# Kernel tuning notes

Hardware: AMD Instinct MI355X
Metric: run time of the kernel (lower is better)

Reference implementation:

```python
import jax, jax.numpy as jnp
import numpy as np

HISTORY = 128  # self-inclusive causal window width

def _layernorm(x, g, b, eps=1e-5):
    mu = jnp.mean(x, axis=-1, keepdims=True)
    var = jnp.var(x, axis=-1, keepdims=True)
    return (x - mu) * jax.lax.rsqrt(var + eps) * g + b

def setup_inputs() -> dict:
    key = jax.random.key(0)
    ks = jax.random.split(key, 8)
    dim, hid, B, T = 64, 256, 4, 4096
    s = lambda fan_in: 1.0 / np.sqrt(fan_in)
    return {
        "x": jax.random.normal(ks[0], (B, T, dim), jnp.float32),
        "W_in": jax.random.normal(ks[1], (dim, hid), jnp.float32) * s(dim),
        "b_in": jnp.zeros((hid,), jnp.float32),
        "W_qkv": jax.random.normal(ks[2], (hid, 3 * hid), jnp.float32) * s(hid),
        "b_qkv": jnp.zeros((3 * hid,), jnp.float32),
        "g_attn": jnp.ones((hid,), jnp.float32),
        "be_attn": jnp.zeros((hid,), jnp.float32),
        "g_mlp": jnp.ones((hid,), jnp.float32),
        "be_mlp": jnp.zeros((hid,), jnp.float32),
        "W1": jax.random.normal(ks[3], (hid, hid), jnp.float32) * s(hid),
        "b1": jnp.zeros((hid,), jnp.float32),
        "W2": jax.random.normal(ks[4], (hid, hid), jnp.float32) * s(hid),
        "b2": jnp.zeros((hid,), jnp.float32),
        "W_out": jax.random.normal(ks[5], (hid, dim), jnp.float32) * s(hid),
        "b_out": jnp.zeros((dim,), jnp.float32),
    }

def reference(x, W_in, b_in, W_qkv, b_qkv, g_attn, be_attn, g_mlp, be_mlp,
              W1, b1, W2, b2, W_out, b_out):
    B, T, _ = x.shape
    hid = W_in.shape[1]
    h = x @ W_in + b_in                                  # (B,T,hid)
    qkv = _layernorm(h, g_attn, be_attn) @ W_qkv + b_qkv
    q, k, v = jnp.split(qkv, 3, axis=-1)
    scale = 1.0 / jnp.sqrt(jnp.asarray(hid, x.dtype))
    scores = jnp.einsum('bqd,bkd->bqk', q, k) * scale    # (B,T,T)
    idx = jnp.arange(T)
    delta = idx[:, None] - idx[None, :]
    mask = (delta >= 0) & (delta <= HISTORY)             # self-inclusive window
    scores = jnp.where(mask[None], scores, jnp.finfo(x.dtype).min)
    attn = jax.nn.softmax(scores, axis=-1)
    attn_out = jnp.einsum('bqk,bkd->bqd', attn, v)
    h = h + attn_out                                     # residual (dropout=0)
    m = _layernorm(h, g_mlp, be_mlp)
    m = jax.nn.gelu(m @ W1 + b1, approximate=False) @ W2 + b2
    h = h + m
    return h @ W_out + b_out                             # (B,T,dim)
```

## Files before the change

kernel.cpp:

```cpp
#include <hip/hip_runtime.h>
#include <hip/hip_bf16.h>
#include <math.h>

typedef short bf8 __attribute__((ext_vector_type(8)));
typedef float f4  __attribute__((ext_vector_type(4)));

#define DEV static __device__ __forceinline__

DEV f4 MFMA(bf8 a, bf8 b, f4 c) { return __builtin_amdgcn_mfma_f32_16x16x32_bf16(a, b, c, 0, 0, 0); }

DEV unsigned short f2bf(float f) {
  union { float f; unsigned int u; } v; v.f = f;
  unsigned int r = v.u + 0x7FFFu + ((v.u >> 16) & 1u);
  return (unsigned short)(r >> 16);
}
DEV float bf2f(unsigned short u) {
  union { unsigned int u; float f; } v; v.u = ((unsigned int)u) << 16;
  return v.f;
}

struct P15 { const void* p[15]; };

DEV float ldin(const void* p, int i, bool bf) {
  return bf ? bf2f(((const unsigned short*)p)[i]) : ((const float*)p)[i];
}

#define PB_IN 0
#define PB_QKV 256
#define PB1 1024
#define PB2 1280
#define PB_OUT 1536
#define PGA 1600
#define PBA 1856
#define PGM 2112
#define PBM 2368

__global__ __launch_bounds__(256) void k_prep(P15 in,
    unsigned short* __restrict__ WinT, unsigned short* __restrict__ WqkvT,
    unsigned short* __restrict__ W1T, unsigned short* __restrict__ W2T,
    unsigned short* __restrict__ WoutT, float* __restrict__ par)
{
  const bool bf = (*(const unsigned int*)in.p[5]) == 0x3F803F80u;
  const int E0 = 16384;
  const int E1 = E0 + 196608;
  const int E2 = E1 + 65536;
  const int E3 = E2 + 65536;
  const int E4 = E3 + 16384;
  const int E5 = E4 + 2624;
  for (int i = blockIdx.x * 256 + threadIdx.x; i < E5; i += gridDim.x * 256) {
    if (i < E0) {
      int n = i >> 6, k = i & 63;
      WinT[i] = f2bf(ldin(in.p[1], k * 256 + n, bf));
    } else if (i < E1) {
      int j = i - E0, n = j >> 8, k = j & 255;
      WqkvT[j] = f2bf(ldin(in.p[3], k * 768 + n, bf));
    } else if (i < E2) {
      int j = i - E1, n = j >> 8, k = j & 255;
      W1T[j] = f2bf(ldin(in.p[9], k * 256 + n, bf));
    } else if (i < E3) {
      int j = i - E2, n = j >> 8, k = j & 255;
      W2T[j] = f2bf(ldin(in.p[11], k * 256 + n, bf));
    } else if (i < E4) {
      int j = i - E3, n = j >> 8, k = j & 255;
      WoutT[j] = f2bf(ldin(in.p[13], k * 64 + n, bf));
    } else {
      int j = i - E4;
      const void* src; int o;
      if (j < 256)       { src = in.p[2];  o = j; }
      else if (j < 1024) { src = in.p[4];  o = j - 256; }
      else if (j < 1280) { src = in.p[10]; o = j - 1024; }
      else if (j < 1536) { src = in.p[12]; o = j - 1280; }
      else if (j < 1600) { src = in.p[14]; o = j - 1536; }
      else if (j < 1856) { src = in.p[5];  o = j - 1600; }
      else if (j < 2112) { src = in.p[6];  o = j - 1856; }
      else if (j < 2368) { src = in.p[7];  o = j - 2112; }
      else               { src = in.p[8];  o = j - 2368; }
      par[j] = ldin(src, o, bf);
    }
  }
}

__global__ __launch_bounds__(512, 2) void k_in_qkv(const void* __restrict__ xin,
    const unsigned short* __restrict__ WinT, const unsigned short* __restrict__ WqkvT,
    const float* __restrict__ par, const void* __restrict__ probe,
    float* __restrict__ h, unsigned short* __restrict__ qb,
    unsigned short* __restrict__ kb, unsigned short* __restrict__ vT)
{
  __shared__ unsigned short smem[33280 + 18432];
  __shared__ float sStat[8][16][2];
  unsigned short* sQK = smem;
  unsigned short* sX  = smem;
  unsigned short* sW  = smem + 4608;
  unsigned short* sLn = smem + 33280;
  unsigned short* sV  = smem + 33280;
  const int tid = threadIdx.x, lane = tid & 63, w = tid >> 6;
  const int l15 = lane & 15, l4 = lane >> 4;
  const int m0 = blockIdx.x * 64;
  const bool bf = (*(const unsigned int*)probe) == 0x3F803F80u;

  {
    int r = tid >> 3, c8 = (tid & 7) * 8;
    if (bf) {
      *(bf8*)&sX[r * 72 + c8] = *(const bf8*)((const unsigned short*)xin + (m0 + r) * 64 + c8);
    } else {
      const float* xf = (const float*)xin + (m0 + r) * 64 + c8;
      float4 f0 = *(const float4*)xf, f1 = *(const float4*)(xf + 4);
      unsigned short t8[8] = { f2bf(f0.x), f2bf(f0.y), f2bf(f0.z), f2bf(f0.w),
                               f2bf(f1.x), f2bf(f1.y), f2bf(f1.z), f2bf(f1.w) };
      *(bf8*)&sX[r * 72 + c8] = *(const bf8*)t8;
    }
  }
  for (int t = tid; t < 2048; t += 512) {
    int r = t >> 3, c8 = (t & 7) * 8;
    *(bf8*)&sW[r * 72 + c8] = *(const bf8*)&WinT[r * 64 + c8];
  }
  __syncthreads();

  const int rm = w & 3, cg = w >> 2;
  f4 z = {0.f, 0.f, 0.f, 0.f};
  f4 acc1[8];
  #pragma unroll
  for (int f = 0; f < 8; ++f) acc1[f] = z;
  bf8 ax0 = *(const bf8*)&sX[(16 * rm + l15) * 72 + l4 * 8];
  bf8 ax1 = *(const bf8*)&sX[(16 * rm + l15) * 72 + 32 + l4 * 8];
  #pragma unroll
  for (int f = 0; f < 8; ++f) {
    bf8 b0 = *(const bf8*)&sW[(128 * cg + 16 * f + l15) * 72 + l4 * 8];
    bf8 b1 = *(const bf8*)&sW[(128 * cg + 16 * f + l15) * 72 + 32 + l4 * 8];
    acc1[f] = MFMA(ax0, b0, acc1[f]);
    acc1[f] = MFMA(ax1, b1, acc1[f]);
  }
  float s[4] = {0,0,0,0}, s2[4] = {0,0,0,0};
  #pragma unroll
  for (int f = 0; f < 8; ++f) {
    float bias = par[PB_IN + 128 * cg + 16 * f + l15];
    #pragma unroll
    for (int r = 0; r < 4; ++r) {
      float v = acc1[f][r] + bias; acc1[f][r] = v;
      s[r] += v; s2[r] += v * v;
    }
  }
  #pragma unroll
  for (int m = 1; m <= 8; m <<= 1) {
    #pragma unroll
    for (int r = 0; r < 4; ++r) { s[r] += __shfl_xor(s[r], m); s2[r] += __shfl_xor(s2[r], m); }
  }
  if (l15 == 0) {
    #pragma unroll
    for (int r = 0; r < 4; ++r) { sStat[w][4 * l4 + r][0] = s[r]; sStat[w][4 * l4 + r][1] = s2[r]; }
  }
  __syncthreads();
  float mu[4], rstd[4];
  #pragma unroll
  for (int r = 0; r < 4; ++r) {
    float st  = s[r]  + sStat[w ^ 4][4 * l4 + r][0];
    float st2 = s2[r] + sStat[w ^ 4][4 * l4 + r][1];
    mu[r] = st * (1.f / 256.f);
    rstd[r] = rsqrtf(st2 * (1.f / 256.f) - mu[r] * mu[r] + 1e-5f);
  }
  #pragma unroll
  for (int f = 0; f < 8; ++f) {
    int col = 128 * cg + 16 * f + l15;
    float g = par[PGA + col], be = par[PBA + col];
    #pragma unroll
    for (int r = 0; r < 4; ++r) {
      int rl = 16 * rm + 4 * l4 + r;
      h[(m0 + rl) * 256 + col] = acc1[f][r];
      sLn[rl * 264 + col] = f2bf((acc1[f][r] - mu[r]) * rstd[r] * g + be);
    }
  }
  __syncthreads();

  const int rm2 = w & 1, cg2 = w >> 1;
  bf8 a2[2][8];
  #pragma unroll
  for (int i = 0; i < 2; ++i)
    #pragma unroll
    for (int ks = 0; ks < 8; ++ks)
      a2[i][ks] = *(const bf8*)&sLn[(32 * rm2 + 16 * i + l15) * 264 + ks * 32 + l4 * 8];
  __syncthreads();
  f4 acc2[2][12];
  #pragma unroll
  for (int i = 0; i < 2; ++i)
    #pragma unroll
    for (int f = 0; f < 12; ++f) acc2[i][f] = z;
  #pragma unroll
  for (int f = 0; f < 12; ++f) {
    const unsigned short* bp = &WqkvT[(192 * cg2 + 16 * f + l15) * 256 + l4 * 8];
    #pragma unroll
    for (int ks = 0; ks < 8; ++ks) {
      bf8 b = *(const bf8*)&bp[ks * 32];
      acc2[0][f] = MFMA(a2[0][ks], b, acc2[0][f]);
      acc2[1][f] = MFMA(a2[1][ks], b, acc2[1][f]);
    }
  }
  #pragma unroll
  for (int i = 0; i < 2; ++i) {
    #pragma unroll
    for (int f = 0; f < 12; ++f) {
      int col = 192 * cg2 + 16 * f + l15;
      float bias = par[PB_QKV + col];
      int rl = 32 * rm2 + 16 * i + 4 * l4;
      #pragma unroll
      for (int r = 0; r < 4; ++r) {
        unsigned short bv = f2bf(acc2[i][f][r] + bias);
        if (col < 512) sQK[(rl + r) * 520 + col] = bv;
        else           sV[(col - 512) * 72 + rl + r] = bv;
      }
    }
  }
  __syncthreads();
  const int bb = m0 >> 12, t0 = m0 & 4095;
  for (int ch = tid; ch < 4096; ch += 512) {
    int r = ch >> 6, c8 = (ch & 63) * 8;
    bf8 v = *(const bf8*)&sQK[r * 520 + c8];
    if (c8 < 256) *(bf8*)&qb[(m0 + r) * 256 + c8] = v;
    else          *(bf8*)&kb[(m0 + r) * 256 + (c8 - 256)] = v;
  }
  for (int ch = tid; ch < 2048; ch += 512) {
    int d = ch >> 3, c8 = (ch & 7) * 8;
    *(bf8*)&vT[(bb * 256 + d) * 4096 + t0 + c8] = *(const bf8*)&sV[d * 72 + c8];
  }
}

__global__ __launch_bounds__(256) void k_attn(const unsigned short* __restrict__ qb,
    const unsigned short* __restrict__ kb, const unsigned short* __restrict__ vT,
    const float* __restrict__ h, const float* __restrict__ par,
    float* __restrict__ h2, unsigned short* __restrict__ ln2)
{
  __shared__ unsigned short sKV[256 * 72];
  __shared__ unsigned short sP[64 * 200];
  const int tid = threadIdx.x, lane = tid & 63, w = tid >> 6;
  const int l15 = lane & 15, l4 = lane >> 4;
  const int b = blockIdx.x >> 6, q0 = (blockIdx.x & 63) * 64;
  const int tok0 = b * 4096 + q0, kstart = q0 - 128;

  bf8 qreg[8];
  {
    const int qrow = tok0 + 16 * w + l15;
    #pragma unroll
    for (int ks = 0; ks < 8; ++ks)
      qreg[ks] = *(const bf8*)&qb[qrow * 256 + ks * 32 + l4 * 8];
  }

  f4 z = {0.f, 0.f, 0.f, 0.f};
  f4 sacc[12];
  #pragma unroll
  for (int i = 0; i < 12; ++i) sacc[i] = z;

  #pragma unroll
  for (int c = 0; c < 3; ++c) {
    for (int t = tid; t < 2048; t += 256) {
      int r = t >> 5, c8 = (t & 31) * 8;
      int j = kstart + 64 * c + r; if (j < 0) j = 0;
      *(bf8*)&sKV[r * 264 + c8] = *(const bf8*)&kb[(b * 4096 + j) * 256 + c8];
    }
    __syncthreads();
    #pragma unroll
    for (int ks = 0; ks < 8; ++ks) {
      #pragma unroll
      for (int fn = 0; fn < 4; ++fn) {
        bf8 bfr = *(const bf8*)&sKV[(16 * fn + l15) * 264 + ks * 32 + l4 * 8];
        sacc[4 * c + fn] = MFMA(qreg[ks], bfr, sacc[4 * c + fn]);
      }
    }
    __syncthreads();
  }

  const float scale = 0.0625f;
  float mx[4] = {-1e30f, -1e30f, -1e30f, -1e30f};
  #pragma unroll
  for (int c = 0; c < 3; ++c) {
    #pragma unroll
    for (int fn = 0; fn < 4; ++fn) {
      int kk = 64 * c + 16 * fn + l15;
      #pragma unroll
      for (int r = 0; r < 4; ++r) {
        int qi = 16 * w + 4 * l4 + r;
        bool valid = (kk >= qi) && (kk <= qi + 128) && (kstart + kk >= 0);
        float sv = valid ? sacc[4 * c + fn][r] * scale : -1e30f;
        sacc[4 * c + fn][r] = sv;
        mx[r] = fmaxf(mx[r], sv);
      }
    }
  }
  #pragma unroll
  for (int msk = 1; msk <= 8; msk <<= 1) {
    #pragma unroll
    for (int r = 0; r < 4; ++r) mx[r] = fmaxf(mx[r], __shfl_xor(mx[r], msk));
  }
  float sum[4] = {0,0,0,0};
  #pragma unroll
  for (int c = 0; c < 3; ++c) {
    #pragma unroll
    for (int fn = 0; fn < 4; ++fn) {
      #pragma unroll
      for (int r = 0; r < 4; ++r) {
        float p = __expf(sacc[4 * c + fn][r] - mx[r]);
        sacc[4 * c + fn][r] = p;
        sum[r] += p;
      }
    }
  }
  #pragma unroll
  for (int msk = 1; msk <= 8; msk <<= 1) {
    #pragma unroll
    for (int r = 0; r < 4; ++r) sum[r] += __shfl_xor(sum[r], msk);
  }
  #pragma unroll
  for (int c = 0; c < 3; ++c) {
    #pragma unroll
    for (int fn = 0; fn < 4; ++fn) {
      #pragma unroll
      for (int r = 0; r < 4; ++r) {
        int kk = 64 * c + 16 * fn + l15;
        sP[(16 * w + 4 * l4 + r) * 200 + kk] = f2bf(sacc[4 * c + fn][r]);
      }
    }
  }

  f4 oacc[16];
  #pragma unroll
  for (int f = 0; f < 16; ++f) oacc[f] = z;
  #pragma unroll
  for (int c = 0; c < 3; ++c) {
    for (int t = tid; t < 2048; t += 256) {
      int d = t >> 3, c8 = (t & 7) * 8;
      int j0 = kstart + 64 * c + c8; if (j0 < 0) j0 = 0;
      *(bf8*)&sKV[d * 72 + c8] = *(const bf8*)&vT[(b * 256 + d) * 4096 + j0];
    }
    __syncthreads();
    #pragma unroll
    for (int ks = 0; ks < 2; ++ks) {
      bf8 a = *(const bf8*)&sP[(16 * w + l15) * 200 + 64 * c + ks * 32 + l4 * 8];
      #pragma unroll
      for (int f = 0; f < 16; ++f) {
        bf8 bv = *(const bf8*)&sKV[(16 * f + l15) * 72 + ks * 32 + l4 * 8];
        oacc[f] = MFMA(a, bv, oacc[f]);
      }
    }
    __syncthreads();
  }

  float inv[4];
  #pragma unroll
  for (int r = 0; r < 4; ++r) inv[r] = 1.f / sum[r];
  float s[4] = {0,0,0,0}, s2[4] = {0,0,0,0};
  #pragma unroll
  for (int f = 0; f < 16; ++f) {
    int col = 16 * f + l15;
    #pragma unroll
    for (int r = 0; r < 4; ++r) {
      int row = tok0 + 16 * w + 4 * l4 + r;
      float v = h[row * 256 + col] + oacc[f][r] * inv[r];
      oacc[f][r] = v; s[r] += v; s2[r] += v * v;
    }
  }
  #pragma unroll
  for (int msk = 1; msk <= 8; msk <<= 1) {
    #pragma unroll
    for (int r = 0; r < 4; ++r) { s[r] += __shfl_xor(s[r], msk); s2[r] += __shfl_xor(s2[r], msk); }
  }
  float mu[4], rstd[4];
  #pragma unroll
  for (int r = 0; r < 4; ++r) {
    mu[r] = s[r] * (1.f / 256.f);
    float var = s2[r] * (1.f / 256.f) - mu[r] * mu[r];
    rstd[r] = rsqrtf(var + 1e-5f);
  }
  #pragma unroll
  for (int f = 0; f < 16; ++f) {
    int col = 16 * f + l15;
    float g = par[PGM + col], be = par[PBM + col];
    #pragma unroll
    for (int r = 0; r < 4; ++r) {
      int row = tok0 + 16 * w + 4 * l4 + r;
      h2[row * 256 + col] = oacc[f][r];
      ln2[row * 256 + col] = f2bf((oacc[f][r] - mu[r]) * rstd[r] * g + be);
    }
  }
}

__global__ __launch_bounds__(512, 2) void k_mlp_out(const unsigned short* __restrict__ ln2,
    const unsigned short* __restrict__ W1T, const unsigned short* __restrict__ W2T,
    const unsigned short* __restrict__ WoutT, const float* __restrict__ par,
    const float* __restrict__ h2, void* __restrict__ dout, const void* __restrict__ probe)
{
  __shared__ unsigned short sL[64 * 264];
  __shared__ unsigned short sM[64 * 264];
  __shared__ unsigned short sH[64 * 264];
  const int tid = threadIdx.x, lane = tid & 63, w = tid >> 6;
  const int l15 = lane & 15, l4 = lane >> 4;
  const int m0 = blockIdx.x * 64;
  const bool obf = (*(const unsigned int*)probe) == 0x3F803F80u;

  for (int t = tid; t < 2048; t += 512) {
    int r = t >> 5, c8 = (t & 31) * 8;
    *(bf8*)&sL[r * 264 + c8] = *(const bf8*)&ln2[(m0 + r) * 256 + c8];
  }
  __syncthreads();
  const int rm2 = w & 1, cg = w >> 1;
  f4 z = {0.f, 0.f, 0.f, 0.f};

  {
    bf8 a[2][8];
    #pragma unroll
    for (int i = 0; i < 2; ++i)
      #pragma unroll
      for (int ks = 0; ks < 8; ++ks)
        a[i][ks] = *(const bf8*)&sL[(32 * rm2 + 16 * i + l15) * 264 + ks * 32 + l4 * 8];
    f4 acc[2][4];
    #pragma unroll
    for (int i = 0; i < 2; ++i)
      #pragma unroll
      for (int f = 0; f < 4; ++f) acc[i][f] = z;
    #pragma unroll
    for (int f = 0; f < 4; ++f) {
      const unsigned short* bp = &W1T[(64 * cg + 16 * f + l15) * 256 + l4 * 8];
      #pragma unroll
      for (int ks = 0; ks < 8; ++ks) {
        bf8 b = *(const bf8*)&bp[ks * 32];
        acc[0][f] = MFMA(a[0][ks], b, acc[0][f]);
        acc[1][f] = MFMA(a[1][ks], b, acc[1][f]);
      }
    }
    #pragma unroll
    for (int i = 0; i < 2; ++i) {
      #pragma unroll
      for (int f = 0; f < 4; ++f) {
        int col = 64 * cg + 16 * f + l15;
        float bias = par[PB1 + col];
        #pragma unroll
        for (int r = 0; r < 4; ++r) {
          float v = acc[i][f][r] + bias;
          float gl = 0.5f * v * (1.0f + erff(v * 0.70710678118654752f));
          sM[(32 * rm2 + 16 * i + 4 * l4 + r) * 264 + col] = f2bf(gl);
        }
      }
    }
  }
  __syncthreads();

  {
    bf8 a[2][8];
    #pragma unroll
    for (int i = 0; i < 2; ++i)
      #pragma unroll
      for (int ks = 0; ks < 8; ++ks)
        a[i][ks] = *(const bf8*)&sM[(32 * rm2 + 16 * i + l15) * 264 + ks * 32 + l4 * 8];
    f4 acc[2][4];
    #pragma unroll
    for (int i = 0; i < 2; ++i)
      #pragma unroll
      for (int f = 0; f < 4; ++f) acc[i][f] = z;
    #pragma unroll
    for (int f = 0; f < 4; ++f) {
      const unsigned short* bp = &W2T[(64 * cg + 16 * f + l15) * 256 + l4 * 8];
      #pragma unroll
      for (int ks = 0; ks < 8; ++ks) {
        bf8 b = *(const bf8*)&bp[ks * 32];
        acc[0][f] = MFMA(a[0][ks], b, acc[0][f]);
        acc[1][f] = MFMA(a[1][ks], b, acc[1][f]);
      }
    }
    #pragma unroll
    for (int i = 0; i < 2; ++i) {
      #pragma unroll
      for (int f = 0; f < 4; ++f) {
        int col = 64 * cg + 16 * f + l15;
        float bias = par[PB2 + col];
        #pragma unroll
        for (int r = 0; r < 4; ++r) {
          int row = 32 * rm2 + 16 * i + 4 * l4 + r;
          float v = h2[(m0 + row) * 256 + col] + acc[i][f][r] + bias;
          sH[row * 264 + col] = f2bf(v);
        }
      }
    }
  }
  __syncthreads();

  {
    bf8 a[2][8];
    #pragma unroll
    for (int i = 0; i < 2; ++i)
      #pragma unroll
      for (int ks = 0; ks < 8; ++ks)
        a[i][ks] = *(const bf8*)&sH[(32 * rm2 + 16 * i + l15) * 264 + ks * 32 + l4 * 8];
    f4 acc[2];
    acc[0] = z; acc[1] = z;
    const unsigned short* bp = &WoutT[(16 * cg + l15) * 256 + l4 * 8];
    #pragma unroll
    for (int ks = 0; ks < 8; ++ks) {
      bf8 b = *(const bf8*)&bp[ks * 32];
      acc[0] = MFMA(a[0][ks], b, acc[0]);
      acc[1] = MFMA(a[1][ks], b, acc[1]);
    }
    int col = 16 * cg + l15;
    float bias = par[PB_OUT + col];
    #pragma unroll
    for (int i = 0; i < 2; ++i) {
      #pragma unroll
      for (int r = 0; r < 4; ++r) {
        int row = m0 + 32 * rm2 + 16 * i + 4 * l4 + r;
        float v = acc[i][r] + bias;
        if (obf) ((unsigned short*)dout)[row * 64 + col] = f2bf(v);
        else     ((float*)dout)[row * 64 + col] = v;
      }
    }
  }
}

extern "C" void kernel_launch(void* const* d_in, const int* in_sizes, int n_in,
                              void* d_out, int out_size, void* d_ws, size_t ws_size,
                              hipStream_t stream)
{
  (void)in_sizes; (void)n_in; (void)out_size; (void)ws_size;
  char* ws = (char*)d_ws;
  size_t off = 0;
  auto A = [&](size_t bytes) { void* p = (void*)(ws + off); off += (bytes + 255) & ~(size_t)255; return p; };

  unsigned short* WinT  = (unsigned short*)A(32768);
  unsigned short* WqkvT = (unsigned short*)A(393216);
  unsigned short* W1T   = (unsigned short*)A(131072);
  unsigned short* W2T   = (unsigned short*)A(131072);
  unsigned short* WoutT = (unsigned short*)A(32768);
  float* par            = (float*)A(10496);
  float* h              = (float*)A(16777216);
  unsigned short* qb    = (unsigned short*)A(8388608);
  unsigned short* kb    = (unsigned short*)A(8388608);
  unsigned short* vT    = (unsigned short*)A(8388608);
  float* h2             = (float*)A(16777216);
  unsigned short* ln2   = (unsigned short*)A(8388608);

  P15 in;
  for (int i = 0; i < 15; ++i) in.p[i] = d_in[i];

  k_prep   <<<dim3(1419), dim3(256), 0, stream>>>(in, WinT, WqkvT, W1T, W2T, WoutT, par);
  k_in_qkv <<<dim3(256),  dim3(512), 0, stream>>>(d_in[0], WinT, WqkvT, par, d_in[5], h, qb, kb, vT);
  k_attn   <<<dim3(256),  dim3(256), 0, stream>>>(qb, kb, vT, h, par, h2, ln2);
  k_mlp_out<<<dim3(256),  dim3(512), 0, stream>>>(ln2, W1T, W2T, WoutT, par, h2, d_out, d_in[5]);
}
```

Measured before the change: 175.7 us.

## Fuse all stages into one cooperative persistent kernel with grid syncs

```diff
diff --git a/kernel.cpp b/kernel.cpp
--- a/kernel.cpp
+++ b/kernel.cpp
@@ -1,6 +1,9 @@
 #include <hip/hip_runtime.h>
+#include <hip/hip_cooperative_groups.h>
 #include <hip/hip_bf16.h>
 #include <math.h>
+
+namespace cg = cooperative_groups;
 
 typedef short bf8 __attribute__((ext_vector_type(8)));
 typedef float f4  __attribute__((ext_vector_type(4)));
@@ -35,75 +38,82 @@
 #define PGM 2112
 #define PBM 2368
 
-__global__ __launch_bounds__(256) void k_prep(P15 in,
+__global__ __launch_bounds__(512, 2) void k_mega(P15 in,
     unsigned short* __restrict__ WinT, unsigned short* __restrict__ WqkvT,
     unsigned short* __restrict__ W1T, unsigned short* __restrict__ W2T,
-    unsigned short* __restrict__ WoutT, float* __restrict__ par)
+    unsigned short* __restrict__ WoutT, float* __restrict__ par,
+    unsigned short* __restrict__ kb, unsigned short* __restrict__ vT,
+    void* __restrict__ dout)
 {
-  const bool bf = (*(const unsigned int*)in.p[5]) == 0x3F803F80u;
-  const int E0 = 16384;
-  const int E1 = E0 + 196608;
-  const int E2 = E1 + 65536;
-  const int E3 = E2 + 65536;
-  const int E4 = E3 + 16384;
-  const int E5 = E4 + 2624;
-  for (int i = blockIdx.x * 256 + threadIdx.x; i < E5; i += gridDim.x * 256) {
-    if (i < E0) {
-      int n = i >> 6, k = i & 63;
-      WinT[i] = f2bf(ldin(in.p[1], k * 256 + n, bf));
-    } else if (i < E1) {
-      int j = i - E0, n = j >> 8, k = j & 255;
-      WqkvT[j] = f2bf(ldin(in.p[3], k * 768 + n, bf));
-    } else if (i < E2) {
-      int j = i - E1, n = j >> 8, k = j & 255;
-      W1T[j] = f2bf(ldin(in.p[9], k * 256 + n, bf));
-    } else if (i < E3) {
-      int j = i - E2, n = j >> 8, k = j & 255;
-      W2T[j] = f2bf(ldin(in.p[11], k * 256 + n, bf));
-    } else if (i < E4) {
-      int j = i - E3, n = j >> 8, k = j & 255;
-      WoutT[j] = f2bf(ldin(in.p[13], k * 64 + n, bf));
-    } else {
-      int j = i - E4;
-      const void* src; int o;
-      if (j < 256)       { src = in.p[2];  o = j; }
-      else if (j < 1024) { src = in.p[4];  o = j - 256; }
-      else if (j < 1280) { src = in.p[10]; o = j - 1024; }
-      else if (j < 1536) { src = in.p[12]; o = j - 1280; }
-      else if (j < 1600) { src = in.p[14]; o = j - 1536; }
-      else if (j < 1856) { src = in.p[5];  o = j - 1600; }
-      else if (j < 2112) { src = in.p[6];  o = j - 1856; }
-      else if (j < 2368) { src = in.p[7];  o = j - 2112; }
-      else               { src = in.p[8];  o = j - 2368; }
-      par[j] = ldin(src, o, bf);
-    }
-  }
-}
-
-__global__ __launch_bounds__(512, 2) void k_in_qkv(const void* __restrict__ xin,
-    const unsigned short* __restrict__ WinT, const unsigned short* __restrict__ WqkvT,
-    const float* __restrict__ par, const void* __restrict__ probe,
-    float* __restrict__ h, unsigned short* __restrict__ qb,
-    unsigned short* __restrict__ kb, unsigned short* __restrict__ vT)
-{
-  __shared__ unsigned short smem[33280 + 18432];
+  __shared__ unsigned short smem[66560];
   __shared__ float sStat[8][16][2];
-  unsigned short* sQK = smem;
-  unsigned short* sX  = smem;
-  unsigned short* sW  = smem + 4608;
-  unsigned short* sLn = smem + 33280;
-  unsigned short* sV  = smem + 33280;
+
   const int tid = threadIdx.x, lane = tid & 63, w = tid >> 6;
   const int l15 = lane & 15, l4 = lane >> 4;
+  const bool bf = (*(const unsigned int*)in.p[5]) == 0x3F803F80u;
+  cg::grid_group grid = cg::this_grid();
+
+  {
+    const int E0 = 16384, E1 = E0 + 196608, E2 = E1 + 65536,
+              E3 = E2 + 65536, E4 = E3 + 16384, E5 = E4 + 2624;
+    for (int i = blockIdx.x * 512 + tid; i < E5; i += gridDim.x * 512) {
+      if (i < E0) {
+        int n = i >> 6, k = i & 63;
+        WinT[i] = f2bf(ldin(in.p[1], k * 256 + n, bf));
+      } else if (i < E1) {
+        int j = i - E0, n = j >> 8, k = j & 255;
+        WqkvT[j] = f2bf(ldin(in.p[3], k * 768 + n, bf));
+      } else if (i < E2) {
+        int j = i - E1, n = j >> 8, k = j & 255;
+        W1T[j] = f2bf(ldin(in.p[9], k * 256 + n, bf));
+      } else if (i < E3) {
+        int j = i - E2, n = j >> 8, k = j & 255;
+        W2T[j] = f2bf(ldin(in.p[11], k * 256 + n, bf));
+      } else if (i < E4) {
+        int j = i - E3, n = j >> 8, k = j & 255;
+        WoutT[j] = f2bf(ldin(in.p[13], k * 64 + n, bf));
+      } else {
+        int j = i - E4;
+        const void* src; int o;
+        if (j < 256)       { src = in.p[2];  o = j; }
+        else if (j < 1024) { src = in.p[4];  o = j - 256; }
+        else if (j < 1280) { src = in.p[10]; o = j - 1024; }
+        else if (j < 1536) { src = in.p[12]; o = j - 1280; }
+        else if (j < 1600) { src = in.p[14]; o = j - 1536; }
+        else if (j < 1856) { src = in.p[5];  o = j - 1600; }
+        else if (j < 2112) { src = in.p[6];  o = j - 1856; }
+        else if (j < 2368) { src = in.p[7];  o = j - 2112; }
+        else               { src = in.p[8];  o = j - 2368; }
+        par[j] = ldin(src, o, bf);
+      }
+    }
+  }
+  grid.sync();
+
   const int m0 = blockIdx.x * 64;
-  const bool bf = (*(const unsigned int*)probe) == 0x3F803F80u;
+  const int bb = m0 >> 12, q0 = m0 & 4095;
+  const int kstart = q0 - 128;
+  const f4 z = {0.f, 0.f, 0.f, 0.f};
+
+  unsigned short* sX   = smem;
+  unsigned short* sW   = smem + 4608;
+  unsigned short* sLn1 = smem + 23040;
+  unsigned short* sKst = smem;
+  unsigned short* sV   = smem + 16896;
+  unsigned short* sQ   = smem + 35328;
+  unsigned short* sKs  = smem;
+  unsigned short* sP   = smem + 18432;
+  unsigned short* sVs  = smem;
+  float*          sh   = (float*)smem;
+  unsigned short* sLn2 = smem + 32768;
+  unsigned short* sM   = smem + 49664;
 
   {
     int r = tid >> 3, c8 = (tid & 7) * 8;
     if (bf) {
-      *(bf8*)&sX[r * 72 + c8] = *(const bf8*)((const unsigned short*)xin + (m0 + r) * 64 + c8);
+      *(bf8*)&sX[r * 72 + c8] = *(const bf8*)((const unsigned short*)in.p[0] + (m0 + r) * 64 + c8);
     } else {
-      const float* xf = (const float*)xin + (m0 + r) * 64 + c8;
+      const float* xf = (const float*)in.p[0] + (m0 + r) * 64 + c8;
       float4 f0 = *(const float4*)xf, f1 = *(const float4*)(xf + 4);
       unsigned short t8[8] = { f2bf(f0.x), f2bf(f0.y), f2bf(f0.z), f2bf(f0.w),
                                f2bf(f1.x), f2bf(f1.y), f2bf(f1.z), f2bf(f1.w) };
@@ -117,395 +127,343 @@
   __syncthreads();
 
   const int rm = w & 3, cg = w >> 2;
-  f4 z = {0.f, 0.f, 0.f, 0.f};
   f4 acc1[8];
   #pragma unroll
   for (int f = 0; f < 8; ++f) acc1[f] = z;
-  bf8 ax0 = *(const bf8*)&sX[(16 * rm + l15) * 72 + l4 * 8];
-  bf8 ax1 = *(const bf8*)&sX[(16 * rm + l15) * 72 + 32 + l4 * 8];
-  #pragma unroll
-  for (int f = 0; f < 8; ++f) {
-    bf8 b0 = *(const bf8*)&sW[(128 * cg + 16 * f + l15) * 72 + l4 * 8];
-    bf8 b1 = *(const bf8*)&sW[(128 * cg + 16 * f + l15) * 72 + 32 + l4 * 8];
-    acc1[f] = MFMA(ax0, b0, acc1[f]);
-    acc1[f] = MFMA(ax1, b1, acc1[f]);
-  }
-  float s[4] = {0,0,0,0}, s2[4] = {0,0,0,0};
-  #pragma unroll
-  for (int f = 0; f < 8; ++f) {
-    float bias = par[PB_IN + 128 * cg + 16 * f + l15];
+  {
+    bf8 ax0 = *(const bf8*)&sX[(16 * rm + l15) * 72 + l4 * 8];
+    bf8 ax1 = *(const bf8*)&sX[(16 * rm + l15) * 72 + 32 + l4 * 8];
+    #pragma unroll
+    for (int f = 0; f < 8; ++f) {
+      bf8 b0 = *(const bf8*)&sW[(128 * cg + 16 * f + l15) * 72 + l4 * 8];
+      bf8 b1 = *(const bf8*)&sW[(128 * cg + 16 * f + l15) * 72 + 32 + l4 * 8];
+      acc1[f] = MFMA(ax0, b0, acc1[f]);
+      acc1[f] = MFMA(ax1, b1, acc1[f]);
+    }
+  }
+  {
+    float s[4] = {0,0,0,0}, s2[4] = {0,0,0,0};
+    #pragma unroll
+    for (int f = 0; f < 8; ++f) {
+      float bias = par[PB_IN + 128 * cg + 16 * f + l15];
+      #pragma unroll
+      for (int r = 0; r < 4; ++r) {
+        float v = acc1[f][r] + bias; acc1[f][r] = v;
+        s[r] += v; s2[r] += v * v;
+      }
+    }
+    #pragma unroll
+    for (int m = 1; m <= 8; m <<= 1) {
+      #pragma unroll
+      for (int r = 0; r < 4; ++r) { s[r] += __shfl_xor(s[r], m); s2[r] += __shfl_xor(s2[r], m); }
+    }
+    if (l15 == 0) {
+      #pragma unroll
+      for (int r = 0; r < 4; ++r) { sStat[w][4 * l4 + r][0] = s[r]; sStat[w][4 * l4 + r][1] = s2[r]; }
+    }
+    __syncthreads();
+    float mu[4], rstd[4];
     #pragma unroll
     for (int r = 0; r < 4; ++r) {
-      float v = acc1[f][r] + bias; acc1[f][r] = v;
-      s[r] += v; s2[r] += v * v;
-    }
-  }
-  #pragma unroll
-  for (int m = 1; m <= 8; m <<= 1) {
-    #pragma unroll
-    for (int r = 0; r < 4; ++r) { s[r] += __shfl_xor(s[r], m); s2[r] += __shfl_xor(s2[r], m); }
-  }
-  if (l15 == 0) {
-    #pragma unroll
-    for (int r = 0; r < 4; ++r) { sStat[w][4 * l4 + r][0] = s[r]; sStat[w][4 * l4 + r][1] = s2[r]; }
-  }
-  __syncthreads();
-  float mu[4], rstd[4];
-  #pragma unroll
-  for (int r = 0; r < 4; ++r) {
-    float st  = s[r]  + sStat[w ^ 4][4 * l4 + r][0];
-    float st2 = s2[r] + sStat[w ^ 4][4 * l4 + r][1];
-    mu[r] = st * (1.f / 256.f);
-    rstd[r] = rsqrtf(st2 * (1.f / 256.f) - mu[r] * mu[r] + 1e-5f);
-  }
-  #pragma unroll
-  for (int f = 0; f < 8; ++f) {
-    int col = 128 * cg + 16 * f + l15;
-    float g = par[PGA + col], be = par[PBA + col];
-    #pragma unroll
-    for (int r = 0; r < 4; ++r) {
-      int rl = 16 * rm + 4 * l4 + r;
-      h[(m0 + rl) * 256 + col] = acc1[f][r];
-      sLn[rl * 264 + col] = f2bf((acc1[f][r] - mu[r]) * rstd[r] * g + be);
-    }
-  }
-  __syncthreads();
-
-  const int rm2 = w & 1, cg2 = w >> 1;
-  bf8 a2[2][8];
-  #pragma unroll
-  for (int i = 0; i < 2; ++i)
-    #pragma unroll
-    for (int ks = 0; ks < 8; ++ks)
-      a2[i][ks] = *(const bf8*)&sLn[(32 * rm2 + 16 * i + l15) * 264 + ks * 32 + l4 * 8];
-  __syncthreads();
-  f4 acc2[2][12];
-  #pragma unroll
-  for (int i = 0; i < 2; ++i)
-    #pragma unroll
-    for (int f = 0; f < 12; ++f) acc2[i][f] = z;
-  #pragma unroll
-  for (int f = 0; f < 12; ++f) {
-    const unsigned short* bp = &WqkvT[(192 * cg2 + 16 * f + l15) * 256 + l4 * 8];
-    #pragma unroll
-    for (int ks = 0; ks < 8; ++ks) {
-      bf8 b = *(const bf8*)&bp[ks * 32];
-      acc2[0][f] = MFMA(a2[0][ks], b, acc2[0][f]);
-      acc2[1][f] = MFMA(a2[1][ks], b, acc2[1][f]);
-    }
-  }
-  #pragma unroll
-  for (int i = 0; i < 2; ++i) {
+      float st  = s[r]  + sStat[w ^ 4][4 * l4 + r][0];
+      float st2 = s2[r] + sStat[w ^ 4][4 * l4 + r][1];
+      mu[r] = st * (1.f / 256.f);
+      rstd[r] = rsqrtf(st2 * (1.f / 256.f) - mu[r] * mu[r] + 1e-5f);
+    }
+    #pragma unroll
+    for (int f = 0; f < 8; ++f) {
+      int col = 128 * cg + 16 * f + l15;
+      float g = par[PGA + col], be = par[PBA + col];
+      #pragma unroll
+      for (int r = 0; r < 4; ++r)
+        sLn1[(16 * rm + 4 * l4 + r) * 264 + col] = f2bf((acc1[f][r] - mu[r]) * rstd[r] * g + be);
+    }
+  }
+  __syncthreads();
+
+  {
+    const int rm2 = w & 1, cg2 = w >> 1;
+    bf8 a2[2][8];
+    #pragma unroll
+    for (int i = 0; i < 2; ++i)
+      #pragma unroll
+      for (int ks = 0; ks < 8; ++ks)
+        a2[i][ks] = *(const bf8*)&sLn1[(32 * rm2 + 16 * i + l15) * 264 + ks * 32 + l4 * 8];
+    __syncthreads();
     #pragma unroll
     for (int f = 0; f < 12; ++f) {
+      f4 acA = z, acB = z;
+      const unsigned short* bp = &WqkvT[(192 * cg2 + 16 * f + l15) * 256 + l4 * 8];
+      #pragma unroll
+      for (int ks = 0; ks < 8; ++ks) {
+        bf8 b = *(const bf8*)&bp[ks * 32];
+        acA = MFMA(a2[0][ks], b, acA);
+        acB = MFMA(a2[1][ks], b, acB);
+      }
       int col = 192 * cg2 + 16 * f + l15;
       float bias = par[PB_QKV + col];
-      int rl = 32 * rm2 + 16 * i + 4 * l4;
-      #pragma unroll
-      for (int r = 0; r < 4; ++r) {
-        unsigned short bv = f2bf(acc2[i][f][r] + bias);
-        if (col < 512) sQK[(rl + r) * 520 + col] = bv;
-        else           sV[(col - 512) * 72 + rl + r] = bv;
-      }
-    }
-  }
-  __syncthreads();
-  const int bb = m0 >> 12, t0 = m0 & 4095;
-  for (int ch = tid; ch < 4096; ch += 512) {
-    int r = ch >> 6, c8 = (ch & 63) * 8;
-    bf8 v = *(const bf8*)&sQK[r * 520 + c8];
-    if (c8 < 256) *(bf8*)&qb[(m0 + r) * 256 + c8] = v;
-    else          *(bf8*)&kb[(m0 + r) * 256 + (c8 - 256)] = v;
+      int rl = 32 * rm2 + 4 * l4;
+      #pragma unroll
+      for (int r = 0; r < 4; ++r) {
+        unsigned short v0 = f2bf(acA[r] + bias);
+        unsigned short v1 = f2bf(acB[r] + bias);
+        if (col < 256)      { sQ[(rl + r) * 264 + col] = v0;          sQ[(rl + 16 + r) * 264 + col] = v1; }
+        else if (col < 512) { sKst[(rl + r) * 264 + col - 256] = v0;  sKst[(rl + 16 + r) * 264 + col - 256] = v1; }
+        else                { sV[(col - 512) * 72 + rl + r] = v0;     sV[(col - 512) * 72 + rl + 16 + r] = v1; }
+      }
+    }
+  }
+  __syncthreads();
+  for (int ch = tid; ch < 2048; ch += 512) {
+    int r = ch >> 5, c8 = (ch & 31) * 8;
+    *(bf8*)&kb[(m0 + r) * 256 + c8] = *(const bf8*)&sKst[r * 264 + c8];
   }
   for (int ch = tid; ch < 2048; ch += 512) {
     int d = ch >> 3, c8 = (ch & 7) * 8;
-    *(bf8*)&vT[(bb * 256 + d) * 4096 + t0 + c8] = *(const bf8*)&sV[d * 72 + c8];
-  }
-}
-
-__global__ __launch_bounds__(256) void k_attn(const unsigned short* __restrict__ qb,
-    const unsigned short* __restrict__ kb, const unsigned short* __restrict__ vT,
-    const float* __restrict__ h, const float* __restrict__ par,
-    float* __restrict__ h2, unsigned short* __restrict__ ln2)
-{
-  __shared__ unsigned short sKV[256 * 72];
-  __shared__ unsigned short sP[64 * 200];
-  const int tid = threadIdx.x, lane = tid & 63, w = tid >> 6;
-  const int l15 = lane & 15, l4 = lane >> 4;
-  const int b = blockIdx.x >> 6, q0 = (blockIdx.x & 63) * 64;
-  const int tok0 = b * 4096 + q0, kstart = q0 - 128;
-
+    *(bf8*)&vT[(bb * 256 + d) * 4096 + q0 + c8] = *(const bf8*)&sV[d * 72 + c8];
+  }
+  grid.sync();
+
+  const int wq = rm, wc = cg;
   bf8 qreg[8];
-  {
-    const int qrow = tok0 + 16 * w + l15;
-    #pragma unroll
-    for (int ks = 0; ks < 8; ++ks)
-      qreg[ks] = *(const bf8*)&qb[qrow * 256 + ks * 32 + l4 * 8];
-  }
-
-  f4 z = {0.f, 0.f, 0.f, 0.f};
-  f4 sacc[12];
-  #pragma unroll
-  for (int i = 0; i < 12; ++i) sacc[i] = z;
-
+  #pragma unroll
+  for (int ks = 0; ks < 8; ++ks)
+    qreg[ks] = *(const bf8*)&sQ[(16 * wq + l15) * 264 + ks * 32 + l4 * 8];
+
+  f4 sacc[6];
+  #pragma unroll
+  for (int i = 0; i < 6; ++i) sacc[i] = z;
   #pragma unroll
   for (int c = 0; c < 3; ++c) {
-    for (int t = tid; t < 2048; t += 256) {
+    for (int t = tid; t < 2048; t += 512) {
       int r = t >> 5, c8 = (t & 31) * 8;
       int j = kstart + 64 * c + r; if (j < 0) j = 0;
-      *(bf8*)&sKV[r * 264 + c8] = *(const bf8*)&kb[(b * 4096 + j) * 256 + c8];
+      *(bf8*)&sKs[r * 264 + c8] = *(const bf8*)&kb[(bb * 4096 + j) * 256 + c8];
     }
     __syncthreads();
     #pragma unroll
     for (int ks = 0; ks < 8; ++ks) {
       #pragma unroll
-      for (int fn = 0; fn < 4; ++fn) {
-        bf8 bfr = *(const bf8*)&sKV[(16 * fn + l15) * 264 + ks * 32 + l4 * 8];
-        sacc[4 * c + fn] = MFMA(qreg[ks], bfr, sacc[4 * c + fn]);
-      }
-    }
-    __syncthreads();
-  }
-
-  const float scale = 0.0625f;
-  float mx[4] = {-1e30f, -1e30f, -1e30f, -1e30f};
+      for (int j2 = 0; j2 < 2; ++j2) {
+        bf8 bk = *(const bf8*)&sKs[(32 * wc + 16 * j2 + l15) * 264 + ks * 32 + l4 * 8];
+        sacc[2 * c + j2] = MFMA(qreg[ks], bk, sacc[2 * c + j2]);
+      }
+    }
+    __syncthreads();
+  }
+
+  float inv[4];
+  {
+    const float scale = 0.0625f;
+    float mx[4] = {-1e30f, -1e30f, -1e30f, -1e30f};
+    #pragma unroll
+    for (int c = 0; c < 3; ++c) {
+      #pragma unroll
+      for (int j2 = 0; j2 < 2; ++j2) {
+        int kk = 64 * c + 32 * wc + 16 * j2 + l15;
+        #pragma unroll
+        for (int r = 0; r < 4; ++r) {
+          int qi = 16 * wq + 4 * l4 + r;
+          bool valid = (kk >= qi) && (kk <= qi + 128) && (kstart + kk >= 0);
+          float sv = valid ? sacc[2 * c + j2][r] * scale : -1e30f;
+          sacc[2 * c + j2][r] = sv;
+          mx[r] = fmaxf(mx[r], sv);
+        }
+      }
+    }
+    #pragma unroll
+    for (int m = 1; m <= 8; m <<= 1) {
+      #pragma unroll
+      for (int r = 0; r < 4; ++r) mx[r] = fmaxf(mx[r], __shfl_xor(mx[r], m));
+    }
+    if (l15 == 0) {
+      #pragma unroll
+      for (int r = 0; r < 4; ++r) sStat[w][4 * l4 + r][0] = mx[r];
+    }
+    __syncthreads();
+    #pragma unroll
+    for (int r = 0; r < 4; ++r) mx[r] = fmaxf(mx[r], sStat[w ^ 4][4 * l4 + r][0]);
+    float sum[4] = {0,0,0,0};
+    #pragma unroll
+    for (int c = 0; c < 3; ++c) {
+      #pragma unroll
+      for (int j2 = 0; j2 < 2; ++j2) {
+        #pragma unroll
+        for (int r = 0; r < 4; ++r) {
+          float p = __expf(sacc[2 * c + j2][r] - mx[r]);
+          sacc[2 * c + j2][r] = p;
+          sum[r] += p;
+        }
+      }
+    }
+    #pragma unroll
+    for (int m = 1; m <= 8; m <<= 1) {
+      #pragma unroll
+      for (int r = 0; r < 4; ++r) sum[r] += __shfl_xor(sum[r], m);
+    }
+    if (l15 == 0) {
+      #pragma unroll
+      for (int r = 0; r < 4; ++r) sStat[w][4 * l4 + r][1] = sum[r];
+    }
+    __syncthreads();
+    #pragma unroll
+    for (int r = 0; r < 4; ++r) inv[r] = 1.f / (sum[r] + sStat[w ^ 4][4 * l4 + r][1]);
+    #pragma unroll
+    for (int c = 0; c < 3; ++c) {
+      #pragma unroll
+      for (int j2 = 0; j2 < 2; ++j2) {
+        int kk = 64 * c + 32 * wc + 16 * j2 + l15;
+        #pragma unroll
+        for (int r = 0; r < 4; ++r)
+          sP[(16 * wq + 4 * l4 + r) * 200 + kk] = f2bf(sacc[2 * c + j2][r]);
+      }
+    }
+  }
+
+  f4 oacc[8];
+  #pragma unroll
+  for (int f = 0; f < 8; ++f) oacc[f] = z;
   #pragma unroll
   for (int c = 0; c < 3; ++c) {
-    #pragma unroll
-    for (int fn = 0; fn < 4; ++fn) {
-      int kk = 64 * c + 16 * fn + l15;
-      #pragma unroll
-      for (int r = 0; r < 4; ++r) {
-        int qi = 16 * w + 4 * l4 + r;
-        bool valid = (kk >= qi) && (kk <= qi + 128) && (kstart + kk >= 0);
-        float sv = valid ? sacc[4 * c + fn][r] * scale : -1e30f;
-        sacc[4 * c + fn][r] = sv;
-        mx[r] = fmaxf(mx[r], sv);
-      }
-    }
-  }
-  #pragma unroll
-  for (int msk = 1; msk <= 8; msk <<= 1) {
-    #pragma unroll
-    for (int r = 0; r < 4; ++r) mx[r] = fmaxf(mx[r], __shfl_xor(mx[r], msk));
-  }
-  float sum[4] = {0,0,0,0};
-  #pragma unroll
-  for (int c = 0; c < 3; ++c) {
-    #pragma unroll
-    for (int fn = 0; fn < 4; ++fn) {
-      #pragma unroll
-      for (int r = 0; r < 4; ++r) {
-        float p = __expf(sacc[4 * c + fn][r] - mx[r]);
-        sacc[4 * c + fn][r] = p;
-        sum[r] += p;
-      }
-    }
-  }
-  #pragma unroll
-  for (int msk = 1; msk <= 8; msk <<= 1) {
-    #pragma unroll
-    for (int r = 0; r < 4; ++r) sum[r] += __shfl_xor(sum[r], msk);
-  }
-  #pragma unroll
-  for (int c = 0; c < 3; ++c) {
-    #pragma unroll
-    for (int fn = 0; fn < 4; ++fn) {
-      #pragma unroll
-      for (int r = 0; r < 4; ++r) {
-        int kk = 64 * c + 16 * fn + l15;
-        sP[(16 * w + 4 * l4 + r) * 200 + kk] = f2bf(sacc[4 * c + fn][r]);
-      }
-    }
-  }
-
-  f4 oacc[16];
-  #pragma unroll
-  for (int f = 0; f < 16; ++f) oacc[f] = z;
-  #pragma unroll
-  for (int c = 0; c < 3; ++c) {
-    for (int t = tid; t < 2048; t += 256) {
+    __syncthreads();
+    for (int t = tid; t < 2048; t += 512) {
       int d = t >> 3, c8 = (t & 7) * 8;
       int j0 = kstart + 64 * c + c8; if (j0 < 0) j0 = 0;
-      *(bf8*)&sKV[d * 72 + c8] = *(const bf8*)&vT[(b * 256 + d) * 4096 + j0];
+      *(bf8*)&sVs[d * 72 + c8] = *(const bf8*)&vT[(bb * 256 + d) * 4096 + j0];
     }
     __syncthreads();
     #pragma unroll
     for (int ks = 0; ks < 2; ++ks) {
-      bf8 a = *(const bf8*)&sP[(16 * w + l15) * 200 + 64 * c + ks * 32 + l4 * 8];
-      #pragma unroll
-      for (int f = 0; f < 16; ++f) {
-        bf8 bv = *(const bf8*)&sKV[(16 * f + l15) * 72 + ks * 32 + l4 * 8];
+      bf8 a = *(const bf8*)&sP[(16 * wq + l15) * 200 + 64 * c + ks * 32 + l4 * 8];
+      #pragma unroll
+      for (int f = 0; f < 8; ++f) {
+        bf8 bv = *(const bf8*)&sVs[(128 * wc + 16 * f + l15) * 72 + ks * 32 + l4 * 8];
         oacc[f] = MFMA(a, bv, oacc[f]);
       }
     }
-    __syncthreads();
-  }
-
-  float inv[4];
-  #pragma unroll
-  for (int r = 0; r < 4; ++r) inv[r] = 1.f / sum[r];
-  float s[4] = {0,0,0,0}, s2[4] = {0,0,0,0};
-  #pragma unroll
-  for (int f = 0; f < 16; ++f) {
-    int col = 16 * f + l15;
+  }
+  __syncthreads();
+
+  {
+    float s[4] = {0,0,0,0}, s2[4] = {0,0,0,0};
+    #pragma unroll
+    for (int f = 0; f < 8; ++f) {
+      #pragma unroll
+      for (int r = 0; r < 4; ++r) {
+        float v = acc1[f][r] + oacc[f][r] * inv[r];
+        acc1[f][r] = v; s[r] += v; s2[r] += v * v;
+      }
+    }
+    #pragma unroll
+    for (int m = 1; m <= 8; m <<= 1) {
+      #pragma unroll
+      for (int r = 0; r < 4; ++r) { s[r] += __shfl_xor(s[r], m); s2[r] += __shfl_xor(s2[r], m); }
+    }
+    if (l15 == 0) {
+      #pragma unroll
+      for (int r = 0; r < 4; ++r) { sStat[w][4 * l4 + r][0] = s[r]; sStat[w][4 * l4 + r][1] = s2[r]; }
+    }
+    __syncthreads();
+    float mu[4], rstd[4];
     #pragma unroll
     for (int r = 0; r < 4; ++r) {
-      int row = tok0 + 16 * w + 4 * l4 + r;
-      float v = h[row * 256 + col] + oacc[f][r] * inv[r];
-      oacc[f][r] = v; s[r] += v; s2[r] += v * v;
-    }
-  }
-  #pragma unroll
-  for (int msk = 1; msk <= 8; msk <<= 1) {
-    #pragma unroll
-    for (int r = 0; r < 4; ++r) { s[r] += __shfl_xor(s[r], msk); s2[r] += __shfl_xor(s2[r], msk); }
-  }
-  float mu[4], rstd[4];
-  #pragma unroll
-  for (int r = 0; r < 4; ++r) {
-    mu[r] = s[r] * (1.f / 256.f);
-    float var = s2[r] * (1.f / 256.f) - mu[r] * mu[r];
-    rstd[r] = rsqrtf(var + 1e-5f);
-  }
-  #pragma unroll
-  for (int f = 0; f < 16; ++f) {
-    int col = 16 * f + l15;
-    float g = par[PGM + col], be = par[PBM + col];
-    #pragma unroll
-    for (int r = 0; r < 4; ++r) {
-      int row = tok0 + 16 * w + 4 * l4 + r;
-      h2[row * 256 + col] = oacc[f][r];
-      ln2[row * 256 + col] = f2bf((oacc[f][r] - mu[r]) * rstd[r] * g + be);
-    }
-  }
-}
-
-__global__ __launch_bounds__(512, 2) void k_mlp_out(const unsigned short* __restrict__ ln2,
-    const unsigned short* __restrict__ W1T, const unsigned short* __restrict__ W2T,
-    const unsigned short* __restrict__ WoutT, const float* __restrict__ par,
-    const float* __restrict__ h2, void* __restrict__ dout, const void* __restrict__ probe)
-{
-  __shared__ unsigned short sL[64 * 264];
-  __shared__ unsigned short sM[64 * 264];
-  __shared__ unsigned short sH[64 * 264];
-  const int tid = threadIdx.x, lane = tid & 63, w = tid >> 6;
-  const int l15 = lane & 15, l4 = lane >> 4;
-  const int m0 = blockIdx.x * 64;
-  const bool obf = (*(const unsigned int*)probe) == 0x3F803F80u;
-
-  for (int t = tid; t < 2048; t += 512) {
-    int r = t >> 5, c8 = (t & 31) * 8;
-    *(bf8*)&sL[r * 264 + c8] = *(const bf8*)&ln2[(m0 + r) * 256 + c8];
-  }
-  __syncthreads();
-  const int rm2 = w & 1, cg = w >> 1;
-  f4 z = {0.f, 0.f, 0.f, 0.f};
-
-  {
-    bf8 a[2][8];
+      float st  = s[r]  + sStat[w ^ 4][4 * l4 + r][0];
+      float st2 = s2[r] + sStat[w ^ 4][4 * l4 + r][1];
+      mu[r] = st * (1.f / 256.f);
+      rstd[r] = rsqrtf(st2 * (1.f / 256.f) - mu[r] * mu[r] + 1e-5f);
+    }
+    #pragma unroll
+    for (int f = 0; f < 8; ++f) {
+      int col = 128 * wc + 16 * f + l15;
+      float g = par[PGM + col], be = par[PBM + col];
+      #pragma unroll
+      for (int r = 0; r < 4; ++r) {
+        int rl = 16 * wq + 4 * l4 + r;
+        sh[rl * 256 + col] = acc1[f][r];
+        sLn2[rl * 264 + col] = f2bf((acc1[f][r] - mu[r]) * rstd[r] * g + be);
+      }
+    }
+  }
+  __syncthreads();
+
+  {
+    const int rm2 = w & 1, cgc = w >> 1;
+    bf8 aC[2][8];
     #pragma unroll
     for (int i = 0; i < 2; ++i)
       #pragma unroll
       for (int ks = 0; ks < 8; ++ks)
-        a[i][ks] = *(const bf8*)&sL[(32 * rm2 + 16 * i + l15) * 264 + ks * 32 + l4 * 8];
-    f4 acc[2][4];
-    #pragma unroll
-    for (int i = 0; i < 2; ++i)
-      #pragma unroll
-      for (int f = 0; f < 4; ++f) acc[i][f] = z;
+        aC[i][ks] = *(const bf8*)&sLn2[(32 * rm2 + 16 * i + l15) * 264 + ks * 32 + l4 * 8];
     #pragma unroll
     for (int f = 0; f < 4; ++f) {
-      const unsigned short* bp = &W1T[(64 * cg + 16 * f + l15) * 256 + l4 * 8];
+      f4 acA = z, acB = z;
+      const unsigned short* bp = &W1T[(64 * cgc + 16 * f + l15) * 256 + l4 * 8];
       #pragma unroll
       for (int ks = 0; ks < 8; ++ks) {
         bf8 b = *(const bf8*)&bp[ks * 32];
-        acc[0][f] = MFMA(a[0][ks], b, acc[0][f]);
-        acc[1][f] = MFMA(a[1][ks], b, acc[1][f]);
-      }
-    }
-    #pragma unroll
-    for (int i = 0; i < 2; ++i) {
-      #pragma unroll
-      for (int f = 0; f < 4; ++f) {
-        int col = 64 * cg + 16 * f + l15;
-        float bias = par[PB1 + col];
-        #pragma unroll
-        for (int r = 0; r < 4; ++r) {
-          float v = acc[i][f][r] + bias;
-          float gl = 0.5f * v * (1.0f + erff(v * 0.70710678118654752f));
-          sM[(32 * rm2 + 16 * i + 4 * l4 + r) * 264 + col] = f2bf(gl);
-        }
-      }
-    }
-  }
-  __syncthreads();
-
-  {
-    bf8 a[2][8];
+        acA = MFMA(aC[0][ks], b, acA);
+        acB = MFMA(aC[1][ks], b, acB);
+      }
+      int col = 64 * cgc + 16 * f + l15;
+      float bias = par[PB1 + col];
+      #pragma unroll
+      for (int r = 0; r < 4; ++r) {
+        float v0 = acA[r] + bias, v1 = acB[r] + bias;
+        sM[(32 * rm2 + 4 * l4 + r) * 264 + col]      = f2bf(0.5f * v0 * (1.0f + erff(v0 * 0.70710678118654752f)));
+        sM[(32 * rm2 + 16 + 4 * l4 + r) * 264 + col] = f2bf(0.5f * v1 * (1.0f + erff(v1 * 0.70710678118654752f)));
+      }
+    }
+    __syncthreads();
+    bf8 aM[2][8];
     #pragma unroll
     for (int i = 0; i < 2; ++i)
       #pragma unroll
       for (int ks = 0; ks < 8; ++ks)
-        a[i][ks] = *(const bf8*)&sM[(32 * rm2 + 16 * i + l15) * 264 + ks * 32 + l4 * 8];
-    f4 acc[2][4];
-    #pragma unroll
-    for (int i = 0; i < 2; ++i)
-      #pragma unroll
-      for (int f = 0; f < 4; ++f) acc[i][f] = z;
+        aM[i][ks] = *(const bf8*)&sM[(32 * rm2 + 16 * i + l15) * 264 + ks * 32 + l4 * 8];
     #pragma unroll
     for (int f = 0; f < 4; ++f) {
-      const unsigned short* bp = &W2T[(64 * cg + 16 * f + l15) * 256 + l4 * 8];
+      f4 acA = z, acB = z;
+      const unsigned short* bp = &W2T[(64 * cgc + 16 * f + l15) * 256 + l4 * 8];
       #pragma unroll
       for (int ks = 0; ks < 8; ++ks) {
         bf8 b = *(const bf8*)&bp[ks * 32];
-        acc[0][f] = MFMA(a[0][ks], b, acc[0][f]);
-        acc[1][f] = MFMA(a[1][ks], b, acc[1][f]);
-      }
-    }
-    #pragma unroll
-    for (int i = 0; i < 2; ++i) {
-      #pragma unroll
-      for (int f = 0; f < 4; ++f) {
-        int col = 64 * cg + 16 * f + l15;
-        float bias = par[PB2 + col];
-        #pragma unroll
-        for (int r = 0; r < 4; ++r) {
-          int row = 32 * rm2 + 16 * i + 4 * l4 + r;
-          float v = h2[(m0 + row) * 256 + col] + acc[i][f][r] + bias;
-          sH[row * 264 + col] = f2bf(v);
-        }
-      }
-    }
-  }
-  __syncthreads();
-
-  {
-    bf8 a[2][8];
-    #pragma unroll
-    for (int i = 0; i < 2; ++i)
-      #pragma unroll
-      for (int ks = 0; ks < 8; ++ks)
-        a[i][ks] = *(const bf8*)&sH[(32 * rm2 + 16 * i + l15) * 264 + ks * 32 + l4 * 8];
-    f4 acc[2];
-    acc[0] = z; acc[1] = z;
-    const unsigned short* bp = &WoutT[(16 * cg + l15) * 256 + l4 * 8];
-    #pragma unroll
-    for (int ks = 0; ks < 8; ++ks) {
-      bf8 b = *(const bf8*)&bp[ks * 32];
-      acc[0] = MFMA(a[0][ks], b, acc[0]);
-      acc[1] = MFMA(a[1][ks], b, acc[1]);
-    }
-    int col = 16 * cg + l15;
-    float bias = par[PB_OUT + col];
-    #pragma unroll
-    for (int i = 0; i < 2; ++i) {
-      #pragma unroll
-      for (int r = 0; r < 4; ++r) {
-        int row = m0 + 32 * rm2 + 16 * i + 4 * l4 + r;
-        float v = acc[i][r] + bias;
-        if (obf) ((unsigned short*)dout)[row * 64 + col] = f2bf(v);
-        else     ((float*)dout)[row * 64 + col] = v;
+        acA = MFMA(aM[0][ks], b, acA);
+        acB = MFMA(aM[1][ks], b, acB);
+      }
+      int col = 64 * cgc + 16 * f + l15;
+      float bias = par[PB2 + col];
+      #pragma unroll
+      for (int r = 0; r < 4; ++r) {
+        int r0 = 32 * rm2 + 4 * l4 + r;
+        sLn2[r0 * 264 + col]        = f2bf(sh[r0 * 256 + col] + acA[r] + bias);
+        sLn2[(r0 + 16) * 264 + col] = f2bf(sh[(r0 + 16) * 256 + col] + acB[r] + bias);
+      }
+    }
+  }
+  __syncthreads();
+  {
+    const int wq3 = w & 3, wc3 = w >> 2;
+    bf8 aO[8];
+    #pragma unroll
+    for (int ks = 0; ks < 8; ++ks)
+      aO[ks] = *(const bf8*)&sLn2[(16 * wq3 + l15) * 264 + ks * 32 + l4 * 8];
+    #pragma unroll
+    for (int j = 0; j < 2; ++j) {
+      f4 acO = z;
+      const unsigned short* bp = &WoutT[(32 * wc3 + 16 * j + l15) * 256 + l4 * 8];
+      #pragma unroll
+      for (int ks = 0; ks < 8; ++ks) {
+        bf8 b = *(const bf8*)&bp[ks * 32];
+        acO = MFMA(aO[ks], b, acO);
+      }
+      int col = 32 * wc3 + 16 * j + l15;
+      float bias = par[PB_OUT + col];
+      #pragma unroll
+      for (int r = 0; r < 4; ++r) {
+        int row = m0 + 16 * wq3 + 4 * l4 + r;
+        float v = acO[r] + bias;
+        if (bf) ((unsigned short*)dout)[row * 64 + col] = f2bf(v);
+        else    ((float*)dout)[row * 64 + col] = v;
       }
     }
   }
@@ -526,18 +484,13 @@
   unsigned short* W2T   = (unsigned short*)A(131072);
   unsigned short* WoutT = (unsigned short*)A(32768);
   float* par            = (float*)A(10496);
-  float* h              = (float*)A(16777216);
-  unsigned short* qb    = (unsigned short*)A(8388608);
   unsigned short* kb    = (unsigned short*)A(8388608);
   unsigned short* vT    = (unsigned short*)A(8388608);
-  float* h2             = (float*)A(16777216);
-  unsigned short* ln2   = (unsigned short*)A(8388608);
 
   P15 in;
   for (int i = 0; i < 15; ++i) in.p[i] = d_in[i];
-
-  k_prep   <<<dim3(1419), dim3(256), 0, stream>>>(in, WinT, WqkvT, W1T, W2T, WoutT, par);
-  k_in_qkv <<<dim3(256),  dim3(512), 0, stream>>>(d_in[0], WinT, WqkvT, par, d_in[5], h, qb, kb, vT);
-  k_attn   <<<dim3(256),  dim3(256), 0, stream>>>(qb, kb, vT, h, par, h2, ln2);
-  k_mlp_out<<<dim3(256),  dim3(512), 0, stream>>>(ln2, W1T, W2T, WoutT, par, h2, d_out, d_in[5]);
+  void* doutv = d_out;
+
+  void* args[] = { &in, &WinT, &WqkvT, &W1T, &W2T, &WoutT, &par, &kb, &vT, &doutv };
+  hipLaunchCooperativeKernel((const void*)k_mega, dim3(256), dim3(512), args, 0, stream);
 }
```

Result: slower. 258.4 us (+47.1%).
